# Optimization experiments

Hardware: AMD Instinct MI355X
Metric: run time of the kernel (lower is better)

Reference implementation:

```python
import jax, jax.numpy as jnp
import numpy as np

H_SIZE = 1024
N_HEADS = 16
HEAD_DIM = H_SIZE // N_HEADS
TAU2 = 1.0
LN_EPS = 1e-5


def setup_inputs() -> dict:
    key = jax.random.key(0)
    ks = jax.random.split(key, 12)
    B, S = 2, 1024
    s = 1.0 / np.sqrt(H_SIZE)
    inp = {
        "input": jax.random.normal(ks[0], (B, S, H_SIZE), dtype=jnp.float32),
        "input_mask": jnp.ones((B, S), dtype=jnp.float32),
        # uniform(0,1) noise; converted to Gumbel(0,1) inside reference
        "gumbel": jax.random.uniform(ks[1], (B, N_HEADS, S, S), dtype=jnp.float32,
                                     minval=1e-10, maxval=1.0),
        "Wq": jax.random.normal(ks[2], (H_SIZE, H_SIZE), dtype=jnp.float32) * s,
        "bq": jnp.zeros((H_SIZE,), dtype=jnp.float32),
        "Wk": jax.random.normal(ks[3], (H_SIZE, H_SIZE), dtype=jnp.float32) * s,
        "bk": jnp.zeros((H_SIZE,), dtype=jnp.float32),
        "Wv": jax.random.normal(ks[4], (H_SIZE, H_SIZE), dtype=jnp.float32) * s,
        "bv": jnp.zeros((H_SIZE,), dtype=jnp.float32),
        "Wo": jax.random.normal(ks[5], (H_SIZE, H_SIZE), dtype=jnp.float32) * s,
        "bo": jnp.zeros((H_SIZE,), dtype=jnp.float32),
        "gamma": jnp.ones((H_SIZE,), dtype=jnp.float32),
        "beta": jnp.zeros((H_SIZE,), dtype=jnp.float32),
    }
    return inp


def reference(input, input_mask, gumbel, Wq, bq, Wk, bk, Wv, bv, Wo, bo, gamma, beta):
    B, S, _ = input.shape
    # projections -> [B, H, S, D]
    def proj(W, b):
        y = jnp.einsum('bsh,oh->bso', input, W) + b  # torch Linear: x @ W.T + b
        return y.reshape(B, S, N_HEADS, HEAD_DIM).transpose(0, 2, 1, 3)
    qq = proj(Wq, bq)
    kk = proj(Wk, bk)
    vv = proj(Wv, bv)
    # raw scores (NOTE: original has no 1/sqrt(d) scaling)
    interact = jnp.einsum('bhqd,bhkd->bhqk', qq, kk)
    # gumbel-softmax (soft): softmax((logits + g)/tau)
    g = -jnp.log(-jnp.log(gumbel))
    sto_attn = jax.nn.softmax((interact + g) / TAU2, axis=-1)
    # masking: mask_1 over query dim, mask_2 over key dim
    mask = input_mask[:, None, :, None] * input_mask[:, None, None, :]  # [B,1,S,S]
    attn = sto_attn * mask
    # (dropout p=0 -> identity)
    out = jnp.einsum('bhqk,bhkd->bhqd', attn, vv)
    out = out.transpose(0, 2, 1, 3).reshape(B, S, H_SIZE)
    out = jnp.einsum('bsh,oh->bso', out, Wo) + bo
    # residual + layernorm
    x = out + input
    mu = jnp.mean(x, axis=-1, keepdims=True)
    var = jnp.mean(jnp.square(x - mu), axis=-1, keepdims=True)
    return (x - mu) * jax.lax.rsqrt(var + LN_EPS) * gamma + beta
```

## Files before the change

kernel.cpp:

```cpp
#include <hip/hip_runtime.h>

#define S_LEN 1024
#define HSZ   1024
#define NHEAD 16
#define HD    64
#define BATCH 2
#define MROWS 2048
#define SOFTMAX_M0 50.0f

typedef unsigned short u16;
typedef __attribute__((ext_vector_type(8))) short short8;
typedef __attribute__((ext_vector_type(4))) short short4v;
typedef __attribute__((ext_vector_type(4))) float f32x4;

#define MFMA_BF16(a, b, c) __builtin_amdgcn_mfma_f32_16x16x32_bf16((a), (b), (c), 0, 0, 0)

__device__ __forceinline__ u16 f2bf(float f) {
    union { float f; unsigned u; } c; c.f = f;
    unsigned u = c.u;
    u += 0x7fffu + ((u >> 16) & 1u);
    return (u16)(u >> 16);
}
__device__ __forceinline__ float bf2f(u16 s) {
    union { unsigned u; float f; } c; c.u = ((unsigned)s) << 16;
    return c.f;
}
__device__ __forceinline__ short8 ld8(const u16* p) {
    return *reinterpret_cast<const short8*>(p);
}
__device__ __forceinline__ void gld16(const u16* g, u16* l) {
    __builtin_amdgcn_global_load_lds(
        (const __attribute__((address_space(1))) unsigned int*)g,
        (__attribute__((address_space(3))) unsigned int*)l, 16, 0, 0);
}
__device__ __forceinline__ int frag_off(int row, int cbb) {
    return (((row << 3) | (cbb ^ (row & 7))) << 3);
}

template<int MT>
__device__ __forceinline__ void gemm_tile(const u16* __restrict__ Ag,
                                          const u16* __restrict__ Bg,
                                          int klen, u16* As, u16* Bs,
                                          f32x4 (&acc)[MT][4]) {
    const int tid  = threadIdx.x;
    const int wave = tid >> 6, lane = tid & 63;
    const int lr = lane & 15, grp = lane >> 4;
    const int wm = wave >> 1, wn = wave & 1;

#pragma unroll
    for (int mt = 0; mt < MT; mt++)
#pragma unroll
        for (int nt = 0; nt < 4; nt++)
            acc[mt][nt] = (f32x4){0.f, 0.f, 0.f, 0.f};

    for (int k0 = 0; k0 < klen; k0 += 64) {
        __syncthreads();
#pragma unroll
        for (int j = 0; j < MT; j++) {
            int c = j * 256 + tid, row = c >> 3, cb = (c & 7) ^ (row & 7);
            gld16(Ag + (size_t)row * HSZ + k0 + cb * 8, As + c * 8);
        }
#pragma unroll
        for (int j = 0; j < 4; j++) {
            int c = j * 256 + tid, row = c >> 3, cb = (c & 7) ^ (row & 7);
            gld16(Bg + (size_t)row * HSZ + k0 + cb * 8, Bs + c * 8);
        }
        __syncthreads();

#pragma unroll
        for (int h = 0; h < 2; h++) {
            const int cbb = h * 4 + grp;
            short8 af[MT], bf[4];
#pragma unroll
            for (int mt = 0; mt < MT; mt++)
                af[mt] = ld8(As + frag_off(wm * (MT * 16) + mt * 16 + lr, cbb));
#pragma unroll
            for (int nt = 0; nt < 4; nt++)
                bf[nt] = ld8(Bs + frag_off(wn * 64 + nt * 16 + lr, cbb));
#pragma unroll
            for (int mt = 0; mt < MT; mt++)
#pragma unroll
                for (int nt = 0; nt < 4; nt++)
                    acc[mt][nt] = MFMA_BF16(af[mt], bf[nt], acc[mt][nt]);
        }
    }
}

__global__ __launch_bounds__(256)
void convert_kernel(const float* __restrict__ x,  const float* __restrict__ wq,
                    const float* __restrict__ wk, const float* __restrict__ wv,
                    const float* __restrict__ wo, u16* __restrict__ dst) {
    const int XV = (MROWS * HSZ) / 4;
    const int WV = (HSZ * HSZ) / 4;
    int vid = blockIdx.x * 256 + threadIdx.x;
    const float* src; int off;
    if (vid < XV)            { src = x;  off = vid; }
    else if (vid < XV + WV)  { src = wq; off = vid - XV; }
    else if (vid < XV + 2*WV){ src = wk; off = vid - XV - WV; }
    else if (vid < XV + 3*WV){ src = wv; off = vid - XV - 2*WV; }
    else                     { src = wo; off = vid - XV - 3*WV; }
    float4 v = reinterpret_cast<const float4*>(src)[off];
    ushort4 o;
    o.x = f2bf(v.x); o.y = f2bf(v.y); o.z = f2bf(v.z); o.w = f2bf(v.w);
    reinterpret_cast<ushort4*>(dst)[vid] = o;
}

__global__ __launch_bounds__(256)
void qkv_gemm(const u16* __restrict__ xb,
              const u16* __restrict__ wqb, const u16* __restrict__ wkb,
              const u16* __restrict__ wvb,
              const float* __restrict__ bq, const float* __restrict__ bk,
              const float* __restrict__ bv, const float* __restrict__ mask,
              u16* __restrict__ qout, u16* __restrict__ kout,
              u16* __restrict__ vtout) {
    __shared__ u16 As[64 * 64];
    __shared__ u16 Bs[128 * 64];
    const int ntile = blockIdx.x;
    const int mtile = blockIdx.y;
    const int p  = ntile >> 3;
    const int m0 = mtile * 64;
    const int nw = (ntile & 7) * 128;
    const u16*  W    = (p == 0) ? wqb : (p == 1) ? wkb : wvb;
    const float* bias = (p == 0) ? bq : (p == 1) ? bk : bv;

    f32x4 acc[2][4];
    gemm_tile<2>(xb + (size_t)m0 * HSZ, W + (size_t)nw * HSZ, HSZ, As, Bs, acc);

    const int wave = threadIdx.x >> 6, lane = threadIdx.x & 63;
    const int lr = lane & 15, grp = lane >> 4;
    const int wm = wave >> 1, wn = wave & 1;
#pragma unroll
    for (int mt = 0; mt < 2; mt++)
#pragma unroll
        for (int nt = 0; nt < 4; nt++)
#pragma unroll
            for (int r = 0; r < 4; r++) {
                int m = m0 + wm * 32 + mt * 16 + grp * 4 + r;
                int o = nw + wn * 64 + nt * 16 + lr;
                float val = acc[mt][nt][r] + bias[o];
                int b = m >> 10, s = m & 1023, hh = o >> 6, d = o & 63;
                if (p == 0)
                    qout[(((size_t)(b * NHEAD + hh)) * S_LEN + s) * HD + d] = f2bf(val);
                else if (p == 1)
                    kout[(((size_t)(b * NHEAD + hh)) * S_LEN + s) * HD + d] = f2bf(val);
                else
                    vtout[(((size_t)(b * NHEAD + hh)) * HD + d) * S_LEN + s] =
                        f2bf(val * mask[m]);
            }
}

__global__ __launch_bounds__(256, 4)
void attn_kernel(const u16* __restrict__ qb, const u16* __restrict__ kb,
                 const u16* __restrict__ vt, const float* __restrict__ gumbel,
                 u16* __restrict__ po, float* __restrict__ pl) {
    const int bh   = blockIdx.y;
    const int qt   = blockIdx.x;
    const int half = blockIdx.z;
    const int q0 = qt * 64, kbase = half * 512;
    const int tid = threadIdx.x;
    const int wave = tid >> 6, lane = tid & 63;
    const int lr = lane & 15, grp = lane >> 4;

    const u16* Q = qb + (size_t)bh * S_LEN * HD;
    const u16* K = kb + (size_t)bh * S_LEN * HD;
    const u16* V = vt + (size_t)bh * HD * S_LEN;
    const int qw = q0 + wave * 16;
    const float* Gp = gumbel + (size_t)bh * S_LEN * S_LEN + (size_t)(qw + lr) * S_LEN;

    __shared__ u16 pbuf[4 * 16 * 68];
    u16* pw = pbuf + wave * (16 * 68);

    short8 aq0 = ld8(Q + (size_t)(qw + lr) * HD + grp * 8);
    short8 aq1 = ld8(Q + (size_t)(qw + lr) * HD + 32 + grp * 8);

    f32x4 acco[4];
#pragma unroll
    for (int i = 0; i < 4; i++) acco[i] = (f32x4){0.f, 0.f, 0.f, 0.f};
    float lsum = 0.f;

    f32x4 gc[4], gn[4];
#pragma unroll
    for (int kt = 0; kt < 4; kt++)
        gc[kt] = *reinterpret_cast<const f32x4*>(Gp + kbase + kt * 16 + grp * 4);

#pragma unroll
    for (int it = 0; it < 8; it++) {
        const int k0 = kbase + it * 64;

        short8 kf[4][2];
#pragma unroll
        for (int kt = 0; kt < 4; kt++) {
            const u16* kp = K + (size_t)(k0 + kt * 16 + lr) * HD + grp * 8;
            kf[kt][0] = ld8(kp);
            kf[kt][1] = ld8(kp + 32);
        }
        short8 vf[4][2];
#pragma unroll
        for (int nt = 0; nt < 4; nt++) {
            const u16* vp = V + (size_t)(nt * 16 + lr) * S_LEN + k0 + grp * 8;
            vf[nt][0] = ld8(vp);
            vf[nt][1] = ld8(vp + 32);
        }
        if (it < 7) {
#pragma unroll
            for (int kt = 0; kt < 4; kt++)
                gn[kt] = *reinterpret_cast<const f32x4*>(Gp + k0 + 64 + kt * 16 + grp * 4);
        }

#pragma unroll
        for (int kt = 0; kt < 4; kt++) {
            f32x4 a = (f32x4){0.f, 0.f, 0.f, 0.f};
            a = MFMA_BF16(kf[kt][0], aq0, a);
            a = MFMA_BF16(kf[kt][1], aq1, a);
            float p[4];
#pragma unroll
            for (int r = 0; r < 4; r++) {
                float w = -__builtin_amdgcn_rcpf(__logf(gc[kt][r]));
                p[r] = __expf(a[r] - SOFTMAX_M0) * w;
                lsum += p[r];
            }
            ushort4 pk;
            pk.x = f2bf(p[0]); pk.y = f2bf(p[1]);
            pk.z = f2bf(p[2]); pk.w = f2bf(p[3]);
            *reinterpret_cast<ushort4*>(pw + lr * 68 + kt * 16 + grp * 4) = pk;
        }

        short8 pa[2];
#pragma unroll
        for (int ks = 0; ks < 2; ks++) {
            const u16* pp = pw + lr * 68 + ks * 32 + grp * 8;
            short4v lo = *reinterpret_cast<const short4v*>(pp);
            short4v hi = *reinterpret_cast<const short4v*>(pp + 4);
            pa[ks] = __builtin_shufflevector(lo, hi, 0, 1, 2, 3, 4, 5, 6, 7);
        }

#pragma unroll
        for (int nt = 0; nt < 4; nt++)
#pragma unroll
            for (int ks = 0; ks < 2; ks++)
                acco[nt] = MFMA_BF16(pa[ks], vf[nt][ks], acco[nt]);

#pragma unroll
        for (int kt = 0; kt < 4; kt++) gc[kt] = gn[kt];
    }

    lsum += __shfl_xor(lsum, 16, 64);
    lsum += __shfl_xor(lsum, 32, 64);

    const int qbase = ((half * 32 + bh) * 16 + qt) * 64 + wave * 16;
    if (lane < 16) pl[qbase + lane] = lsum;

    const int qidx = qbase + grp * 4;
#pragma unroll
    for (int nt = 0; nt < 4; nt++)
#pragma unroll
        for (int r = 0; r < 4; r++)
            po[(size_t)(qidx + r) * 64 + nt * 16 + lr] = f2bf(acco[nt][r]);
}

__global__ __launch_bounds__(256)
void combine_kernel(const u16* __restrict__ po, const float* __restrict__ pl,
                    const float* __restrict__ mask, u16* __restrict__ ctx) {
    const int qt = blockIdx.x, bh = blockIdx.y;
    const int b = bh >> 4, h = bh & 15;
    const int q = threadIdx.x >> 2;
    const int dc = (threadIdx.x & 3) * 16;
    const int i0 = ((0 * 32 + bh) * 16 + qt) * 64 + q;
    const int i1 = ((1 * 32 + bh) * 16 + qt) * 64 + q;
    float l = pl[i0] + pl[i1];
    float mq = mask[b * S_LEN + qt * 64 + q] / l;
    u16* dst = ctx + ((size_t)(b * S_LEN + qt * 64 + q)) * HSZ + h * 64 + dc;
#pragma unroll
    for (int c = 0; c < 2; c++) {
        short8 a = ld8(po + (size_t)i0 * 64 + dc + c * 8);
        short8 bm = ld8(po + (size_t)i1 * 64 + dc + c * 8);
        short8 o;
#pragma unroll
        for (int j = 0; j < 8; j++)
            o[j] = (short)f2bf((bf2f((u16)a[j]) + bf2f((u16)bm[j])) * mq);
        *reinterpret_cast<short8*>(dst + c * 8) = o;
    }
}

__global__ __launch_bounds__(256)
void oproj_gemm(const u16* __restrict__ A, const u16* __restrict__ W,
                float* __restrict__ part0, float* __restrict__ part1) {
    __shared__ u16 As[64 * 64];
    __shared__ u16 Bs[128 * 64];
    const int ntile = blockIdx.x;
    const int mtile = blockIdx.y;
    const int z     = blockIdx.z;
    const int m0 = mtile * 64, n0 = ntile * 128, koff = z * 512;

    f32x4 acc[2][4];
    gemm_tile<2>(A + (size_t)m0 * HSZ + koff, W + (size_t)n0 * HSZ + koff,
                 512, As, Bs, acc);

    float* dst = z ? part1 : part0;
    const int wave = threadIdx.x >> 6, lane = threadIdx.x & 63;
    const int lr = lane & 15, grp = lane >> 4;
    const int wm = wave >> 1, wn = wave & 1;
#pragma unroll
    for (int mt = 0; mt < 2; mt++)
#pragma unroll
        for (int nt = 0; nt < 4; nt++)
#pragma unroll
            for (int r = 0; r < 4; r++) {
                int m = m0 + wm * 32 + mt * 16 + grp * 4 + r;
                int o = n0 + wn * 64 + nt * 16 + lr;
                dst[(size_t)m * HSZ + o] = acc[mt][nt][r];
            }
}

__global__ __launch_bounds__(256)
void ln_kernel(const float* __restrict__ part0, const float* __restrict__ part1,
               const float* __restrict__ xin, const float* __restrict__ bo,
               const float* __restrict__ gamma, const float* __restrict__ beta,
               float* __restrict__ out) {
    const int row = blockIdx.x;
    const int tid = threadIdx.x;
    const size_t base = (size_t)row * (HSZ / 4);

    float4 p0 = reinterpret_cast<const float4*>(part0)[base + tid];
    float4 p1 = reinterpret_cast<const float4*>(part1)[base + tid];
    float4 xr = reinterpret_cast<const float4*>(xin)[base + tid];
    float4 bb = reinterpret_cast<const float4*>(bo)[tid];
    float4 v;
    v.x = p0.x + p1.x + xr.x + bb.x;
    v.y = p0.y + p1.y + xr.y + bb.y;
    v.z = p0.z + p1.z + xr.z + bb.z;
    v.w = p0.w + p1.w + xr.w + bb.w;

    float s  = v.x + v.y + v.z + v.w;
    float ss = v.x * v.x + v.y * v.y + v.z * v.z + v.w * v.w;
#pragma unroll
    for (int off = 1; off < 64; off <<= 1) {
        s  += __shfl_xor(s, off, 64);
        ss += __shfl_xor(ss, off, 64);
    }
    __shared__ float red[8];
    int wave = tid >> 6, lane = tid & 63;
    if (lane == 0) { red[wave] = s; red[4 + wave] = ss; }
    __syncthreads();
    s  = red[0] + red[1] + red[2] + red[3];
    ss = red[4] + red[5] + red[6] + red[7];
    float mu  = s * (1.f / HSZ);
    float var = ss * (1.f / HSZ) - mu * mu;
    float rstd = rsqrtf(var + 1e-5f);

    float4 g  = reinterpret_cast<const float4*>(gamma)[tid];
    float4 be = reinterpret_cast<const float4*>(beta)[tid];
    float4 o;
    o.x = (v.x - mu) * rstd * g.x + be.x;
    o.y = (v.y - mu) * rstd * g.y + be.y;
    o.z = (v.z - mu) * rstd * g.z + be.z;
    o.w = (v.w - mu) * rstd * g.w + be.w;
    reinterpret_cast<float4*>(out)[base + tid] = o;
}

extern "C" void kernel_launch(void* const* d_in, const int* in_sizes, int n_in,
                              void* d_out, int out_size, void* d_ws, size_t ws_size,
                              hipStream_t stream) {
    (void)in_sizes; (void)n_in; (void)out_size; (void)ws_size;
    const float* x     = (const float*)d_in[0];
    const float* mask  = (const float*)d_in[1];
    const float* gum   = (const float*)d_in[2];
    const float* Wq    = (const float*)d_in[3];
    const float* bq    = (const float*)d_in[4];
    const float* Wk    = (const float*)d_in[5];
    const float* bk    = (const float*)d_in[6];
    const float* Wv    = (const float*)d_in[7];
    const float* bv    = (const float*)d_in[8];
    const float* Wo    = (const float*)d_in[9];
    const float* bo    = (const float*)d_in[10];
    const float* gamma = (const float*)d_in[11];
    const float* beta  = (const float*)d_in[12];
    float* out = (float*)d_out;

    u16* xb  = (u16*)d_ws;
    u16* wqb = xb  + 2097152;
    u16* wkb = wqb + 1048576;
    u16* wvb = wkb + 1048576;
    u16* wob = wvb + 1048576;
    u16* qb  = wob + 1048576;
    u16* kb  = qb  + 2097152;
    u16* vt  = kb  + 2097152;
    u16* ctx = vt  + 2097152;
    float* part0 = (float*)(ctx + 2097152);
    float* pl    = (float*)((char*)part0 + 8388608);
    u16*   po    = xb;
    float* part1 = (float*)xb;

    convert_kernel<<<dim3(6144), dim3(256), 0, stream>>>(x, Wq, Wk, Wv, Wo, xb);
    qkv_gemm<<<dim3(24, 32), dim3(256), 0, stream>>>(xb, wqb, wkb, wvb,
                                                     bq, bk, bv, mask,
                                                     qb, kb, vt);
    attn_kernel<<<dim3(16, 32, 2), dim3(256), 0, stream>>>(qb, kb, vt, gum, po, pl);
    combine_kernel<<<dim3(16, 32), dim3(256), 0, stream>>>(po, pl, mask, ctx);
    oproj_gemm<<<dim3(8, 32, 2), dim3(256), 0, stream>>>(ctx, wob, part0, part1);
    ln_kernel<<<dim3(2048), dim3(256), 0, stream>>>(part0, part1, x, bo,
                                                    gamma, beta, out);
}
```

Measured before the change: 335.4 us.

## Stage K and V tiles in shared memory via direct global-to-LDS loads

Each block now cooperatively loads the 64x64 K and V tiles for an iteration into XOR-swizzled shared memory using direct global-to-LDS loads, and every wave reads its MFMA fragments from there. Before, each of the four waves fetched the same K and V fragments from global memory itself. This cuts redundant global and L2 traffic by four, but adds two block barriers per iteration and disables unrolling of the outer loop, which may reduce overlap of loads with compute.

```diff
diff --git a/kernel.cpp b/kernel.cpp
--- a/kernel.cpp
+++ b/kernel.cpp
@@ -167,6 +167,8 @@
     const int qw = q0 + wave * 16;
     const float* Gp = gumbel + (size_t)bh * S_LEN * S_LEN + (size_t)(qw + lr) * S_LEN;
 
+    __shared__ u16 Ks[64 * 64];
+    __shared__ u16 Vs[64 * 64];
     __shared__ u16 pbuf[4 * 16 * 68];
     u16* pw = pbuf + wave * (16 * 68);
 
@@ -183,35 +185,37 @@
     for (int kt = 0; kt < 4; kt++)
         gc[kt] = *reinterpret_cast<const f32x4*>(Gp + kbase + kt * 16 + grp * 4);
 
-#pragma unroll
+#pragma unroll 1
     for (int it = 0; it < 8; it++) {
         const int k0 = kbase + it * 64;
 
-        short8 kf[4][2];
+        __syncthreads();
+#pragma unroll
+        for (int j = 0; j < 2; j++) {
+            int c = j * 256 + tid, row = c >> 3, cb = (c & 7) ^ (row & 7);
+            gld16(K + (size_t)(k0 + row) * HD + cb * 8, Ks + c * 8);
+        }
+#pragma unroll
+        for (int j = 0; j < 2; j++) {
+            int c = j * 256 + tid, row = c >> 3, cb = (c & 7) ^ (row & 7);
+            gld16(V + (size_t)row * S_LEN + k0 + cb * 8, Vs + c * 8);
+        }
+        __syncthreads();
+
+        if (it < 7) {
+#pragma unroll
+            for (int kt = 0; kt < 4; kt++)
+                gn[kt] = *reinterpret_cast<const f32x4*>(
+                             Gp + k0 + 64 + kt * 16 + grp * 4);
+        }
+
 #pragma unroll
         for (int kt = 0; kt < 4; kt++) {
-            const u16* kp = K + (size_t)(k0 + kt * 16 + lr) * HD + grp * 8;
-            kf[kt][0] = ld8(kp);
-            kf[kt][1] = ld8(kp + 32);
-        }
-        short8 vf[4][2];
-#pragma unroll
-        for (int nt = 0; nt < 4; nt++) {
-            const u16* vp = V + (size_t)(nt * 16 + lr) * S_LEN + k0 + grp * 8;
-            vf[nt][0] = ld8(vp);
-            vf[nt][1] = ld8(vp + 32);
-        }
-        if (it < 7) {
-#pragma unroll
-            for (int kt = 0; kt < 4; kt++)
-                gn[kt] = *reinterpret_cast<const f32x4*>(Gp + k0 + 64 + kt * 16 + grp * 4);
-        }
-
-#pragma unroll
-        for (int kt = 0; kt < 4; kt++) {
+            short8 kf0 = ld8(Ks + frag_off(kt * 16 + lr, grp));
+            short8 kf1 = ld8(Ks + frag_off(kt * 16 + lr, 4 + grp));
             f32x4 a = (f32x4){0.f, 0.f, 0.f, 0.f};
-            a = MFMA_BF16(kf[kt][0], aq0, a);
-            a = MFMA_BF16(kf[kt][1], aq1, a);
+            a = MFMA_BF16(kf0, aq0, a);
+            a = MFMA_BF16(kf1, aq1, a);
             float p[4];
 #pragma unroll
             for (int r = 0; r < 4; r++) {
@@ -238,10 +242,14 @@
         for (int nt = 0; nt < 4; nt++)
 #pragma unroll
             for (int ks = 0; ks < 2; ks++)
-                acco[nt] = MFMA_BF16(pa[ks], vf[nt][ks], acco[nt]);
-
-#pragma unroll
-        for (int kt = 0; kt < 4; kt++) gc[kt] = gn[kt];
+                acco[nt] = MFMA_BF16(pa[ks],
+                                     ld8(Vs + frag_off(nt * 16 + lr, ks * 4 + grp)),
+                                     acco[nt]);
+
+        if (it < 7) {
+#pragma unroll
+            for (int kt = 0; kt < 4; kt++) gc[kt] = gn[kt];
+        }
     }
 
     lsum += __shfl_xor(lsum, 16, 64);
```

Result: faster. 286.0 us (-14.7%).
